# Optimization experiments

Measured on AMD Instinct MI355X. Metric: run time of the kernel, lower is better.

## Reference

```python
import jax, jax.numpy as jnp
import numpy as np

SEQ_LEN = 4096
N_FEAT = 2048
N_PADD = 128


def setup_inputs() -> dict:
    key = jax.random.key(0)
    kx, kw = jax.random.split(key)
    x = jax.random.normal(kx, (SEQ_LEN, N_FEAT), dtype=jnp.float32)
    # Fused QKV dense: features = 3 * n_feat
    W = jax.random.normal(kw, (N_FEAT, 3 * N_FEAT), dtype=jnp.float32) * (1.0 / np.sqrt(N_FEAT))
    b = jnp.zeros((3 * N_FEAT,), dtype=jnp.float32)
    return {"x": x, "W": W, "b": b, "n_padd": N_PADD}


def reference(x, W, b, n_padd):
    # Fused QKV projection, split along feature axis (as in nn.Dense + jnp.split)
    qkv = x @ W + b  # [S, 3F]
    q, k, v = jnp.split(qkv, 3, axis=1)  # each [S, F]
    S, F = q.shape
    idx = jnp.arange(S)
    # scores[i, j] = q_i . k_j / sqrt(F)
    scores = (q @ k.T) * (1.0 / jnp.sqrt(jnp.float32(F)))  # [S, S]
    seq_mask = idx >= n_padd                      # valid (non-padding) positions
    causal = idx[None, :] <= idx[:, None]         # j <= i
    mask = causal & seq_mask[None, :]             # kernel: causal_mask & seq_mask
    row_valid = seq_mask                          # rows < n_padd are not computed/stored
    neg_inf = jnp.float32(-jnp.inf)
    scores = jnp.where(mask, scores, neg_inf)
    # Fully-masked (padding) rows would softmax to NaN; neutralize then zero output.
    scores = jnp.where(row_valid[:, None], scores, 0.0)
    att = jax.nn.softmax(scores, axis=-1)         # row-wise stable softmax
    out = att @ v                                 # [S, F]
    out = jnp.where(row_valid[:, None], out, 0.0)  # padded rows produce zeros
    return out
```

## Files before the change

### kernel.cpp

```cpp
#include <hip/hip_runtime.h>
#include <cstdint>
#include <cstddef>

typedef unsigned short u16;
typedef short v8s __attribute__((ext_vector_type(8)));
typedef float v4f __attribute__((ext_vector_type(4)));

constexpr int SEQ = 4096;
constexpr int FEAT = 2048;
constexpr int F3 = 6144;


__device__ __forceinline__ u16 f2bf(float f) {
  union { float f; uint32_t u; } v; v.f = f;
  uint32_t r = v.u + 0x7FFFu + ((v.u >> 16) & 1u);
  return (u16)(r >> 16);
}

__device__ __forceinline__ float bf2f(u16 s) {
  union { uint32_t u; float f; } v; v.u = ((uint32_t)s) << 16;
  return v.f;
}

__device__ __forceinline__ void gld_lds16(const u16* g, u16* l) {
  __builtin_amdgcn_global_load_lds(
      (const __attribute__((address_space(1))) void*)g,
      (__attribute__((address_space(3))) void*)l, 16, 0, 0);
}


__global__ void cvt_f32_bf16(const float* __restrict__ in, u16* __restrict__ out, int n8) {
  int i = blockIdx.x * 256 + threadIdx.x;
  if (i >= n8) return;
  const float4* p = (const float4*)in + (size_t)i * 2;
  float4 a = p[0], b = p[1];
  union { u16 s[8]; uint4 v; } u;
  u.s[0] = f2bf(a.x); u.s[1] = f2bf(a.y); u.s[2] = f2bf(a.z); u.s[3] = f2bf(a.w);
  u.s[4] = f2bf(b.x); u.s[5] = f2bf(b.y); u.s[6] = f2bf(b.z); u.s[7] = f2bf(b.w);
  *(uint4*)(out + (size_t)i * 8) = u.v;
}

__global__ void transp_f2b(const float* __restrict__ in, int ldin,
                           u16* __restrict__ out, int ldout) {
  __shared__ float tile[32][33];
  int c0 = blockIdx.x * 32, r0 = blockIdx.y * 32;
  int tx = threadIdx.x, ty = threadIdx.y;
#pragma unroll
  for (int p = 0; p < 4; ++p)
    tile[ty + 8 * p][tx] = in[(size_t)(r0 + ty + 8 * p) * ldin + c0 + tx];
  __syncthreads();
#pragma unroll
  for (int p = 0; p < 4; ++p)
    out[(size_t)(c0 + ty + 8 * p) * ldout + r0 + tx] = f2bf(tile[tx][ty + 8 * p]);
}

__global__ void transp_b2b(const u16* __restrict__ in, int ldin,
                           u16* __restrict__ out, int ldout) {
  __shared__ u16 tile[32][33];
  int c0 = blockIdx.x * 32, r0 = blockIdx.y * 32;
  int tx = threadIdx.x, ty = threadIdx.y;
#pragma unroll
  for (int p = 0; p < 4; ++p)
    tile[ty + 8 * p][tx] = in[(size_t)(r0 + ty + 8 * p) * ldin + c0 + tx];
  __syncthreads();
#pragma unroll
  for (int p = 0; p < 4; ++p)
    out[(size_t)(c0 + ty + 8 * p) * ldout + r0 + tx] = tile[tx][ty + 8 * p];
}

template<int OUTBF, int ADDB, int MODE>
__global__ __launch_bounds__(256) void gemm_bt(
    const u16* __restrict__ A, int lda,
    const u16* __restrict__ B, int ldb,
    void* __restrict__ Cv, int ldc,
    int K, const float* __restrict__ bias, float scale) {
  int bi, bj, ks, ke;
  if (MODE == 1) {
    const int t = blockIdx.x;
    bi = (int)((sqrtf(8.f * t + 1.f) - 1.f) * 0.5f);
    while ((bi + 1) * (bi + 2) / 2 <= t) ++bi;
    while (bi * (bi + 1) / 2 > t) --bi;
    bj = t - bi * (bi + 1) / 2;
    const int half = K >> 1;
    ks = blockIdx.z * half; ke = ks + half;
    Cv = (void*)((u16*)Cv + (size_t)blockIdx.z * SEQ * SEQ);
  } else if (MODE == 2) {
    bi = blockIdx.y; bj = blockIdx.x;
    const int half = (bi + 1) * 64;
    ks = blockIdx.z * half; ke = ks + half;
  } else {
    bi = blockIdx.y; bj = blockIdx.x;
    ks = 0; ke = K;
  }
  const int i0 = bi * 128, j0 = bj * 128;

  __shared__ u16 As[128 * 64];
  __shared__ u16 Bs[128 * 64];

  const int t = threadIdx.x;
  const int w = t >> 6, l = t & 63;
  const int wr = w >> 1, wc = w & 1;
  const int lm = l & 15, lq = l >> 4;
  const int lqs = ((lq + (lm >> 1)) & 3) * 8;

  v4f acc[4][4];
#pragma unroll
  for (int a = 0; a < 4; ++a)
#pragma unroll
    for (int b = 0; b < 4; ++b)
      acc[a][b] = v4f{0.f, 0.f, 0.f, 0.f};

  const int c1 = t + 256;
  const int r0c = t >> 2, o0 = ((((t & 3) - ((t >> 3) & 3)) & 3)) * 8;
  const int r1c = c1 >> 2, o1 = ((((c1 & 3) - ((c1 >> 3) & 3)) & 3)) * 8;
  const u16* Ag0 = A + (size_t)(i0 + r0c) * lda + o0;
  const u16* Ag1 = A + (size_t)(i0 + r1c) * lda + o1;
  const u16* Bg0 = B + (size_t)(j0 + r0c) * ldb + o0;
  const u16* Bg1 = B + (size_t)(j0 + r1c) * ldb + o1;
  u16* Al0 = &As[w * 512];
  u16* Al1 = &As[w * 512 + 2048];
  u16* Bl0 = &Bs[w * 512];
  u16* Bl1 = &Bs[w * 512 + 2048];

  for (int k0 = ks; k0 < ke; k0 += 64) {
    gld_lds16(Ag0 + k0, Al0);
    gld_lds16(Ag1 + k0, Al1);
    gld_lds16(Bg0 + k0, Bl0);
    gld_lds16(Bg1 + k0, Bl1);
    gld_lds16(Ag0 + k0 + 32, Al0 + 4096);
    gld_lds16(Ag1 + k0 + 32, Al1 + 4096);
    gld_lds16(Bg0 + k0 + 32, Bl0 + 4096);
    gld_lds16(Bg1 + k0 + 32, Bl1 + 4096);
    __syncthreads();

#pragma unroll
    for (int s = 0; s < 2; ++s) {
      v8s af[4], bfr[4];
#pragma unroll
      for (int mi = 0; mi < 4; ++mi)
        af[mi] = *(const v8s*)&As[s * 4096 + (wr * 64 + mi * 16 + lm) * 32 + lqs];
#pragma unroll
      for (int ni = 0; ni < 4; ++ni)
        bfr[ni] = *(const v8s*)&Bs[s * 4096 + (wc * 64 + ni * 16 + lm) * 32 + lqs];
#pragma unroll
      for (int mi = 0; mi < 4; ++mi)
#pragma unroll
        for (int ni = 0; ni < 4; ++ni)
          acc[mi][ni] = __builtin_amdgcn_mfma_f32_16x16x32_bf16(af[mi], bfr[ni], acc[mi][ni], 0, 0, 0);
    }
    __syncthreads();
  }

#pragma unroll
  for (int mi = 0; mi < 4; ++mi) {
#pragma unroll
    for (int ni = 0; ni < 4; ++ni) {
      const int cc = j0 + wc * 64 + ni * 16 + lm;
      const float badd = ADDB ? bias[cc] : 0.f;
#pragma unroll
      for (int r = 0; r < 4; ++r) {
        const int rr = i0 + wr * 64 + mi * 16 + lq * 4 + r;
        float v = acc[mi][ni][r] * scale + badd;
        if (OUTBF)           ((u16*)Cv)[(size_t)rr * ldc + cc] = f2bf(v);
        else if (MODE == 2)  atomicAdd((float*)Cv + (size_t)rr * ldc + cc, v);
        else                 ((float*)Cv)[(size_t)rr * ldc + cc] = v;
      }
    }
  }
}

__global__ __launch_bounds__(256) void softmax_rows(
    const u16* __restrict__ S0, const u16* __restrict__ S1,
    u16* __restrict__ att, const int* __restrict__ npad_p) {
  const int i = blockIdx.x;
  const int np = *npad_p;
  const int kend = ((i >> 7) + 1) << 7;
  const u16* r0 = S0 + (size_t)i * SEQ;
  const u16* r1 = S1 + (size_t)i * SEQ;
  u16* arow = att + (size_t)i * SEQ;
  const int t = threadIdx.x;

  float m = -3.0e38f, s = 0.f;
  for (int j = np + t; j <= i; j += 256) {
    float v = bf2f(r0[j]) + bf2f(r1[j]);
    if (v > m) { s = s * __expf(m - v) + 1.f; m = v; }
    else       { s += __expf(v - m); }
  }
#pragma unroll
  for (int off = 32; off > 0; off >>= 1) {
    float mo = __shfl_xor(m, off);
    float so = __shfl_xor(s, off);
    float M = fmaxf(m, mo);
    s = s * __expf(m - M) + so * __expf(mo - M);
    m = M;
  }
  __shared__ float sm[4], ss[4];
  const int w = t >> 6, l = t & 63;
  if (l == 0) { sm[w] = m; ss[w] = s; }
  __syncthreads();
  const float M = fmaxf(fmaxf(sm[0], sm[1]), fmaxf(sm[2], sm[3]));
  const float Ssum = ss[0] * __expf(sm[0] - M) + ss[1] * __expf(sm[1] - M) +
                     ss[2] * __expf(sm[2] - M) + ss[3] * __expf(sm[3] - M);
  const float inv = 1.f / Ssum;

  for (int j0b = t * 8; j0b < kend; j0b += 2048) {
    union { u16 s8[8]; uint4 v; } u;
#pragma unroll
    for (int q = 0; q < 8; ++q) {
      const int j = j0b + q;
      float a = 0.f;
      if (j >= np && j <= i)
        a = __expf(bf2f(r0[j]) + bf2f(r1[j]) - M) * inv;
      u.s8[q] = f2bf(a);
    }
    *(uint4*)(arow + j0b) = u.v;
  }
}


extern "C" void kernel_launch(void* const* d_in, const int* in_sizes, int n_in,
                              void* d_out, int out_size, void* d_ws, size_t ws_size,
                              hipStream_t stream) {
  const float* x = (const float*)d_in[0];
  const float* W = (const float*)d_in[1];
  const float* b = (const float*)d_in[2];
  const int* npad = (const int*)d_in[3];
  float* out = (float*)d_out;

  char* p = (char*)d_ws;
  u16* xb = (u16*)p;
  u16* Wt = (u16*)(p + (size_t)SEQ * FEAT * 2);
  u16* att = (u16*)p;
  p += (size_t)SEQ * FEAT * 2 + (size_t)F3 * FEAT * 2;
  u16* qkvb = (u16*)p;  p += (size_t)SEQ * F3 * 2;
  u16* vt   = (u16*)p;  p += (size_t)FEAT * SEQ * 2;
  u16* sc0  = (u16*)p;  p += (size_t)SEQ * SEQ * 2;
  u16* sc1  = (u16*)p;  p += (size_t)SEQ * SEQ * 2;
  if (ws_size < (size_t)(p - (char*)d_ws)) return;

  const float scale = 0.02209708691207961f;

  hipMemsetAsync(d_out, 0, (size_t)SEQ * FEAT * sizeof(float), stream);

  cvt_f32_bf16<<<SEQ * FEAT / 8 / 256, 256, 0, stream>>>(x, xb, SEQ * FEAT / 8);
  transp_f2b<<<dim3(F3 / 32, FEAT / 32), dim3(32, 8), 0, stream>>>(W, F3, Wt, FEAT);
  gemm_bt<1, 1, 0><<<dim3(F3 / 128, SEQ / 128), 256, 0, stream>>>(
      xb, FEAT, Wt, FEAT, (void*)qkvb, F3, FEAT, b, 1.0f);
  transp_b2b<<<dim3(FEAT / 32, SEQ / 32), dim3(32, 8), 0, stream>>>(
      qkvb + 2 * FEAT, F3, vt, SEQ);
  gemm_bt<1, 0, 1><<<dim3(32 * 33 / 2, 1, 2), 256, 0, stream>>>(
      qkvb, F3, qkvb + FEAT, F3, (void*)sc0, SEQ, FEAT, nullptr, scale);
  softmax_rows<<<SEQ, 256, 0, stream>>>(sc0, sc1, att, npad);
  gemm_bt<0, 0, 2><<<dim3(FEAT / 128, SEQ / 128, 2), 256, 0, stream>>>(
      att, SEQ, vt, SEQ, (void*)out, FEAT, 0, nullptr, 1.0f);
}
```

Measured before the change: 410.2 us.

## Add 256x256 pipelined GEMM for QKV projection and full QK^T scores

Introduces a 512-thread 256x256-tile GEMM with double-buffered direct-to-LDS loads, interleaved barriers, MFMA priority raising and partial vmcnt waits. It replaces the 128-tile kernel for both the QKV projection and the score computation. The score GEMM now computes the full 4096x4096 square in one pass over K, instead of the lower-triangle tiles split into two K halves. That removes the second score buffer and the summing in softmax, at the cost of computing the masked upper triangle.

New measurement: 406.0 us. Within noise of the previous version (-1.0%).

```diff
diff --git a/kernel.cpp b/kernel.cpp
--- a/kernel.cpp
+++ b/kernel.cpp
@@ -75,16 +75,7 @@
     void* __restrict__ Cv, int ldc,
     int K, const float* __restrict__ bias, float scale) {
   int bi, bj, ks, ke;
-  if (MODE == 1) {
-    const int t = blockIdx.x;
-    bi = (int)((sqrtf(8.f * t + 1.f) - 1.f) * 0.5f);
-    while ((bi + 1) * (bi + 2) / 2 <= t) ++bi;
-    while (bi * (bi + 1) / 2 > t) --bi;
-    bj = t - bi * (bi + 1) / 2;
-    const int half = K >> 1;
-    ks = blockIdx.z * half; ke = ks + half;
-    Cv = (void*)((u16*)Cv + (size_t)blockIdx.z * SEQ * SEQ);
-  } else if (MODE == 2) {
+  if (MODE == 2) {
     bi = blockIdx.y; bj = blockIdx.x;
     const int half = (bi + 1) * 64;
     ks = blockIdx.z * half; ke = ks + half;
@@ -169,20 +160,161 @@
   }
 }
 
+
+#define BAR()   asm volatile("s_barrier" ::: "memory")
+#define LGKM0() asm volatile("s_waitcnt lgkmcnt(0)" ::: "memory")
+#define VMC6()  asm volatile("s_waitcnt vmcnt(6)" ::: "memory")
+
+#define LDA(BUF, MH) do { _Pragma("unroll") \
+  for (int fi = 0; fi < 4; ++fi) { \
+    const u16* ap = &As[BUF][wr][(MH) * 4096 + fi * 1024]; \
+    af[fi][0] = *(const v8s*)(ap + off0); \
+    af[fi][1] = *(const v8s*)(ap + off1); \
+  } } while (0)
+
+#define LDB(BUF) do { _Pragma("unroll") \
+  for (int ni = 0; ni < 4; ++ni) { \
+    const u16* bp = &Bs[BUF][bh][bo + ni * 1024]; \
+    bfr[ni][0] = *(const v8s*)(bp + off0); \
+    bfr[ni][1] = *(const v8s*)(bp + off1); \
+  } } while (0)
+
+#define MMA(MH, NL) do { _Pragma("unroll") \
+  for (int fi = 0; fi < 4; ++fi) { _Pragma("unroll") \
+    for (int nn = 0; nn < 2; ++nn) { \
+      acc[(MH)*4+fi][(NL)+nn] = __builtin_amdgcn_mfma_f32_16x16x32_bf16( \
+          af[fi][0], bfr[(NL)+nn][0], acc[(MH)*4+fi][(NL)+nn], 0, 0, 0); \
+      acc[(MH)*4+fi][(NL)+nn] = __builtin_amdgcn_mfma_f32_16x16x32_bf16( \
+          af[fi][1], bfr[(NL)+nn][1], acc[(MH)*4+fi][(NL)+nn], 0, 0, 0); \
+    } } } while (0)
+
+#define STG_A(BUF, H, KO) do { \
+  gld_lds16(Ag + (size_t)(H) * 128 * lda + (KO), &As[BUF][H][w * 1024]); \
+  gld_lds16(Ag + ((size_t)(H) * 128 + 8) * lda + (KO), &As[BUF][H][w * 1024 + 512]); \
+  } while (0)
+
+#define STG_B(BUF, H, KO) do { \
+  gld_lds16(Bg + (size_t)(H) * 128 * ldb + (KO), &Bs[BUF][H][w * 1024]); \
+  gld_lds16(Bg + ((size_t)(H) * 128 + 8) * ldb + (KO), &Bs[BUF][H][w * 1024 + 512]); \
+  } while (0)
+
+template<int ADDB>
+__global__ __launch_bounds__(512, 2) void gemm256(
+    const u16* __restrict__ A, int lda,
+    const u16* __restrict__ B, int ldb,
+    u16* __restrict__ C, int ldc,
+    int K, const float* __restrict__ bias, float scale) {
+  const int i0 = blockIdx.y * 256, j0 = blockIdx.x * 256;
+
+  __shared__ u16 As[2][2][8192];
+  __shared__ u16 Bs[2][2][8192];
+
+  const int t = threadIdx.x;
+  const int w = t >> 6, l = t & 63;
+  const int wr = w >> 2, wc = w & 3;
+  const int lm = l & 15, lq = l >> 4;
+  const int bh = wc >> 1, bo = (wc & 1) * 4096;
+
+  const int off0 = lm * 64 + ((lq + lm) & 7) * 8;
+  const int off1 = lm * 64 + ((lq + lm + 4) & 7) * 8;
+
+  const int srow = w * 16 + (l >> 3);
+  const int scol = (((l & 7) - (l >> 3)) & 7) * 8;
+  const u16* Ag = A + (size_t)(i0 + srow) * lda + scol;
+  const u16* Bg = B + (size_t)(j0 + srow) * ldb + scol;
+
+  v4f acc[8][4];
+#pragma unroll
+  for (int a = 0; a < 8; ++a)
+#pragma unroll
+    for (int b = 0; b < 4; ++b)
+      acc[a][b] = v4f{0.f, 0.f, 0.f, 0.f};
+
+  v8s af[4][2], bfr[4][2];
+
+  STG_B(0, 0, 0); STG_B(0, 1, 0); STG_A(0, 0, 0); STG_A(0, 1, 0);
+  STG_B(1, 0, 64); STG_B(1, 1, 64); STG_A(1, 0, 64);
+  VMC6(); BAR();
+
+  const int nit = K >> 7;
+  for (int it = 0; it < nit; ++it) {
+    const int kc = it << 7;
+    const int k1 = kc + 64;
+    int k2 = kc + 128; if (k2 >= K) k2 = 0;
+    int k3 = kc + 192; if (k3 >= K) k3 = 0;
+
+    LDA(0, 0); LDB(0);
+    STG_A(1, 1, k1);
+    BAR(); LGKM0();
+    __builtin_amdgcn_s_setprio(1); MMA(0, 0); __builtin_amdgcn_s_setprio(0);
+    BAR();
+    STG_B(0, 0, k2);
+    BAR();
+    __builtin_amdgcn_s_setprio(1); MMA(0, 2); __builtin_amdgcn_s_setprio(0);
+    BAR();
+    LDA(0, 1);
+    STG_B(0, 1, k2);
+    BAR(); LGKM0();
+    __builtin_amdgcn_s_setprio(1); MMA(1, 0); __builtin_amdgcn_s_setprio(0);
+    BAR();
+    STG_A(0, 0, k2);
+    BAR();
+    __builtin_amdgcn_s_setprio(1); MMA(1, 2); __builtin_amdgcn_s_setprio(0);
+    VMC6(); BAR();
+    LDA(1, 0); LDB(1);
+    STG_A(0, 1, k2);
+    BAR(); LGKM0();
+    __builtin_amdgcn_s_setprio(1); MMA(0, 0); __builtin_amdgcn_s_setprio(0);
+    BAR();
+    STG_B(1, 0, k3);
+    BAR();
+    __builtin_amdgcn_s_setprio(1); MMA(0, 2); __builtin_amdgcn_s_setprio(0);
+    BAR();
+    LDA(1, 1);
+    STG_B(1, 1, k3);
+    BAR(); LGKM0();
+    __builtin_amdgcn_s_setprio(1); MMA(1, 0); __builtin_amdgcn_s_setprio(0);
+    BAR();
+    STG_A(1, 0, k3);
+    BAR();
+    __builtin_amdgcn_s_setprio(1); MMA(1, 2); __builtin_amdgcn_s_setprio(0);
+    VMC6(); BAR();
+  }
+
+#pragma unroll
+  for (int mi = 0; mi < 8; ++mi) {
+#pragma unroll
+    for (int ni = 0; ni < 4; ++ni) {
+      const int cc = j0 + wc * 64 + ni * 16 + lm;
+      const float badd = ADDB ? bias[cc] : 0.f;
+#pragma unroll
+      for (int r = 0; r < 4; ++r) {
+        const int rr = i0 + wr * 128 + mi * 16 + lq * 4 + r;
+        C[(size_t)rr * ldc + cc] = f2bf(acc[mi][ni][r] * scale + badd);
+      }
+    }
+  }
+}
+
+#undef LDA
+#undef LDB
+#undef MMA
+#undef STG_A
+#undef STG_B
+
 __global__ __launch_bounds__(256) void softmax_rows(
-    const u16* __restrict__ S0, const u16* __restrict__ S1,
+    const u16* __restrict__ S0,
     u16* __restrict__ att, const int* __restrict__ npad_p) {
   const int i = blockIdx.x;
   const int np = *npad_p;
   const int kend = ((i >> 7) + 1) << 7;
   const u16* r0 = S0 + (size_t)i * SEQ;
-  const u16* r1 = S1 + (size_t)i * SEQ;
   u16* arow = att + (size_t)i * SEQ;
   const int t = threadIdx.x;
 
   float m = -3.0e38f, s = 0.f;
   for (int j = np + t; j <= i; j += 256) {
-    float v = bf2f(r0[j]) + bf2f(r1[j]);
+    float v = bf2f(r0[j]);
     if (v > m) { s = s * __expf(m - v) + 1.f; m = v; }
     else       { s += __expf(v - m); }
   }
@@ -210,7 +342,7 @@
       const int j = j0b + q;
       float a = 0.f;
       if (j >= np && j <= i)
-        a = __expf(bf2f(r0[j]) + bf2f(r1[j]) - M) * inv;
+        a = __expf(bf2f(r0[j]) - M) * inv;
       u.s8[q] = f2bf(a);
     }
     *(uint4*)(arow + j0b) = u.v;
@@ -235,7 +367,6 @@
   u16* qkvb = (u16*)p;  p += (size_t)SEQ * F3 * 2;
   u16* vt   = (u16*)p;  p += (size_t)FEAT * SEQ * 2;
   u16* sc0  = (u16*)p;  p += (size_t)SEQ * SEQ * 2;
-  u16* sc1  = (u16*)p;  p += (size_t)SEQ * SEQ * 2;
   if (ws_size < (size_t)(p - (char*)d_ws)) return;
 
   const float scale = 0.02209708691207961f;
@@ -244,13 +375,13 @@
 
   cvt_f32_bf16<<<SEQ * FEAT / 8 / 256, 256, 0, stream>>>(x, xb, SEQ * FEAT / 8);
   transp_f2b<<<dim3(F3 / 32, FEAT / 32), dim3(32, 8), 0, stream>>>(W, F3, Wt, FEAT);
-  gemm_bt<1, 1, 0><<<dim3(F3 / 128, SEQ / 128), 256, 0, stream>>>(
-      xb, FEAT, Wt, FEAT, (void*)qkvb, F3, FEAT, b, 1.0f);
+  gemm256<1><<<dim3(F3 / 256, SEQ / 256), 512, 0, stream>>>(
+      xb, FEAT, Wt, FEAT, qkvb, F3, FEAT, b, 1.0f);
   transp_b2b<<<dim3(FEAT / 32, SEQ / 32), dim3(32, 8), 0, stream>>>(
       qkvb + 2 * FEAT, F3, vt, SEQ);
-  gemm_bt<1, 0, 1><<<dim3(32 * 33 / 2, 1, 2), 256, 0, stream>>>(
-      qkvb, F3, qkvb + FEAT, F3, (void*)sc0, SEQ, FEAT, nullptr, scale);
-  softmax_rows<<<SEQ, 256, 0, stream>>>(sc0, sc1, att, npad);
+  gemm256<0><<<dim3(SEQ / 256, SEQ / 256), 512, 0, stream>>>(
+      qkvb, F3, qkvb + FEAT, F3, sc0, SEQ, FEAT, nullptr, scale);
+  softmax_rows<<<SEQ, 256, 0, stream>>>(sc0, att, npad);
   gemm_bt<0, 0, 2><<<dim3(FEAT / 128, SEQ / 128, 2), 256, 0, stream>>>(
       att, SEQ, vt, SEQ, (void*)out, FEAT, 0, nullptr, 1.0f);
 }
```

## Replace GEMM with 128x256 triple-buffered pipelined kernel and drop split-K scores

Applied to the files above, without the earlier changes.

The GEMM kernel is replaced by a 512-thread, 128x256-tile version. It uses a three-stage LDS ring buffer, issues the next global-to-LDS loads before the MFMAs, and waits with explicit vmcnt waits and barriers instead of full syncthreads. It also raises wave priority around the MFMA block and remaps workgroups with a swizzle. The score GEMM now computes the full square in one pass without triangle skipping or split-K, so softmax reads a single score buffer. The trade-off is roughly double the score GEMM work in exchange for better pipelining and larger tiles, and the causal PV split reverses row order across the two halves for balance.

New measurement: 410.1 us. No clear change (-0.0%).

```diff
diff --git a/kernel.cpp b/kernel.cpp
--- a/kernel.cpp
+++ b/kernel.cpp
@@ -68,87 +68,90 @@
     out[(size_t)(c0 + ty + 8 * p) * ldout + r0 + tx] = tile[tx][ty + 8 * p];
 }
 
-template<int OUTBF, int ADDB, int MODE>
-__global__ __launch_bounds__(256) void gemm_bt(
-    const u16* __restrict__ A, int lda,
-    const u16* __restrict__ B, int ldb,
-    void* __restrict__ Cv, int ldc,
-    int K, const float* __restrict__ bias, float scale) {
-  int bi, bj, ks, ke;
-  if (MODE == 1) {
-    const int t = blockIdx.x;
-    bi = (int)((sqrtf(8.f * t + 1.f) - 1.f) * 0.5f);
-    while ((bi + 1) * (bi + 2) / 2 <= t) ++bi;
-    while (bi * (bi + 1) / 2 > t) --bi;
-    bj = t - bi * (bi + 1) / 2;
-    const int half = K >> 1;
-    ks = blockIdx.z * half; ke = ks + half;
-    Cv = (void*)((u16*)Cv + (size_t)blockIdx.z * SEQ * SEQ);
-  } else if (MODE == 2) {
-    bi = blockIdx.y; bj = blockIdx.x;
-    const int half = (bi + 1) * 64;
-    ks = blockIdx.z * half; ke = ks + half;
-  } else {
-    bi = blockIdx.y; bj = blockIdx.x;
-    ks = 0; ke = K;
-  }
-  const int i0 = bi * 128, j0 = bj * 128;
-
-  __shared__ u16 As[128 * 64];
-  __shared__ u16 Bs[128 * 64];
+
+#define BAR()  asm volatile("s_barrier" ::: "memory")
+#define VMC3() asm volatile("s_waitcnt vmcnt(3)" ::: "memory")
+
+template<int LDA, int LDB, int LDC, int OUTMODE ,
+         int ADDB, int CAUSAL, int SWZ>
+__global__ __launch_bounds__(512, 4) void gemmw(
+    const u16* __restrict__ A, const u16* __restrict__ B,
+    void* __restrict__ Cv, int K,
+    const float* __restrict__ bias, float scale) {
+  int bi, bj;
+  if (SWZ) {
+    const int gx = gridDim.x;
+    const int nwg = gx * gridDim.y;
+    const int b = blockIdx.y * gx + blockIdx.x;
+    const int cpx = nwg >> 3;
+    const int s = (b & 7) * cpx + (b >> 3);
+    bj = s % gx;  bi = s / gx;
+  } else { bj = blockIdx.x; bi = blockIdx.y; }
+  int ks, ke;
+  if (CAUSAL) {
+    if (blockIdx.z) bi = (int)gridDim.y - 1 - bi;
+    const int kq = (bi + 1) * 64;
+    ks = blockIdx.z ? kq : 0;  ke = ks + kq;
+  } else { ks = 0; ke = K; }
+  const int i0 = bi * 128, j0 = bj * 256;
+
+  __shared__ u16 As[3][4096];
+  __shared__ u16 Bs[3][8192];
 
   const int t = threadIdx.x;
   const int w = t >> 6, l = t & 63;
-  const int wr = w >> 1, wc = w & 1;
+  const int wr = w >> 2, wc = w & 3;
   const int lm = l & 15, lq = l >> 4;
   const int lqs = ((lq + (lm >> 1)) & 3) * 8;
 
+  const int srow = t >> 2;
+  const int scol = (((t & 3) - ((t >> 3) & 3)) & 3) * 8;
+  const u16* Ag = A + (size_t)(i0 + srow) * LDA + scol;
+  const u16* Bg = B + (size_t)(j0 + srow) * LDB + scol;
+  u16* Al = &As[0][0] + w * 512;
+  u16* Bl = &Bs[0][0] + w * 512;
+
   v4f acc[4][4];
 #pragma unroll
   for (int a = 0; a < 4; ++a)
 #pragma unroll
-    for (int b = 0; b < 4; ++b)
-      acc[a][b] = v4f{0.f, 0.f, 0.f, 0.f};
-
-  const int c1 = t + 256;
-  const int r0c = t >> 2, o0 = ((((t & 3) - ((t >> 3) & 3)) & 3)) * 8;
-  const int r1c = c1 >> 2, o1 = ((((c1 & 3) - ((c1 >> 3) & 3)) & 3)) * 8;
-  const u16* Ag0 = A + (size_t)(i0 + r0c) * lda + o0;
-  const u16* Ag1 = A + (size_t)(i0 + r1c) * lda + o1;
-  const u16* Bg0 = B + (size_t)(j0 + r0c) * ldb + o0;
-  const u16* Bg1 = B + (size_t)(j0 + r1c) * ldb + o1;
-  u16* Al0 = &As[w * 512];
-  u16* Al1 = &As[w * 512 + 2048];
-  u16* Bl0 = &Bs[w * 512];
-  u16* Bl1 = &Bs[w * 512 + 2048];
-
-  for (int k0 = ks; k0 < ke; k0 += 64) {
-    gld_lds16(Ag0 + k0, Al0);
-    gld_lds16(Ag1 + k0, Al1);
-    gld_lds16(Bg0 + k0, Bl0);
-    gld_lds16(Bg1 + k0, Bl1);
-    gld_lds16(Ag0 + k0 + 32, Al0 + 4096);
-    gld_lds16(Ag1 + k0 + 32, Al1 + 4096);
-    gld_lds16(Bg0 + k0 + 32, Bl0 + 4096);
-    gld_lds16(Bg1 + k0 + 32, Bl1 + 4096);
-    __syncthreads();
-
-#pragma unroll
-    for (int s = 0; s < 2; ++s) {
-      v8s af[4], bfr[4];
-#pragma unroll
-      for (int mi = 0; mi < 4; ++mi)
-        af[mi] = *(const v8s*)&As[s * 4096 + (wr * 64 + mi * 16 + lm) * 32 + lqs];
+    for (int b2 = 0; b2 < 4; ++b2)
+      acc[a][b2] = v4f{0.f, 0.f, 0.f, 0.f};
+
+  gld_lds16(Ag + ks, Al);
+  gld_lds16(Bg + ks, Bl);
+  gld_lds16(Bg + 128 * LDB + ks, Bl + 4096);
+  gld_lds16(Ag + ks + 32, Al + 4096);
+  gld_lds16(Bg + ks + 32, Bl + 8192);
+  gld_lds16(Bg + 128 * LDB + ks + 32, Bl + 8192 + 4096);
+  VMC3(); BAR();
+
+  const int nt = (ke - ks) >> 5;
+  int bufr = 0;
+  int k2 = ks + 64;
+  for (int tt = 0; tt < nt; ++tt) {
+    v8s af[4], bf4[4];
+    const u16* Ar = &As[0][0] + bufr * 4096 + (wr * 64 + lm) * 32 + lqs;
+    const u16* Br = &Bs[0][0] + bufr * 8192 + (wc * 64 + lm) * 32 + lqs;
+#pragma unroll
+    for (int mi = 0; mi < 4; ++mi) af[mi] = *(const v8s*)(Ar + mi * 512);
+#pragma unroll
+    for (int ni = 0; ni < 4; ++ni) bf4[ni] = *(const v8s*)(Br + ni * 512);
+    const int sb = (bufr + 2 >= 3) ? bufr - 1 : bufr + 2;
+    const int kst = (k2 < ke) ? k2 : ks;
+    gld_lds16(Ag + kst, Al + sb * 4096);
+    gld_lds16(Bg + kst, Bl + sb * 8192);
+    gld_lds16(Bg + 128 * LDB + kst, Bl + sb * 8192 + 4096);
+    __builtin_amdgcn_s_setprio(1);
+#pragma unroll
+    for (int mi = 0; mi < 4; ++mi)
 #pragma unroll
       for (int ni = 0; ni < 4; ++ni)
-        bfr[ni] = *(const v8s*)&Bs[s * 4096 + (wc * 64 + ni * 16 + lm) * 32 + lqs];
-#pragma unroll
-      for (int mi = 0; mi < 4; ++mi)
-#pragma unroll
-        for (int ni = 0; ni < 4; ++ni)
-          acc[mi][ni] = __builtin_amdgcn_mfma_f32_16x16x32_bf16(af[mi], bfr[ni], acc[mi][ni], 0, 0, 0);
-    }
-    __syncthreads();
+        acc[mi][ni] = __builtin_amdgcn_mfma_f32_16x16x32_bf16(af[mi], bf4[ni], acc[mi][ni], 0, 0, 0);
+    __builtin_amdgcn_s_setprio(0);
+    VMC3(); BAR();
+    bufr = (bufr == 2) ? 0 : bufr + 1;
+    k2 += 32;
   }
 
 #pragma unroll
@@ -160,29 +163,28 @@
 #pragma unroll
       for (int r = 0; r < 4; ++r) {
         const int rr = i0 + wr * 64 + mi * 16 + lq * 4 + r;
-        float v = acc[mi][ni][r] * scale + badd;
-        if (OUTBF)           ((u16*)Cv)[(size_t)rr * ldc + cc] = f2bf(v);
-        else if (MODE == 2)  atomicAdd((float*)Cv + (size_t)rr * ldc + cc, v);
-        else                 ((float*)Cv)[(size_t)rr * ldc + cc] = v;
+        if (OUTMODE == 0)
+          ((u16*)Cv)[(size_t)rr * LDC + cc] = f2bf(acc[mi][ni][r] * scale + badd);
+        else
+          atomicAdd((float*)Cv + (size_t)rr * LDC + cc, acc[mi][ni][r]);
       }
     }
   }
 }
 
 __global__ __launch_bounds__(256) void softmax_rows(
-    const u16* __restrict__ S0, const u16* __restrict__ S1,
+    const u16* __restrict__ S0,
     u16* __restrict__ att, const int* __restrict__ npad_p) {
   const int i = blockIdx.x;
   const int np = *npad_p;
   const int kend = ((i >> 7) + 1) << 7;
   const u16* r0 = S0 + (size_t)i * SEQ;
-  const u16* r1 = S1 + (size_t)i * SEQ;
   u16* arow = att + (size_t)i * SEQ;
   const int t = threadIdx.x;
 
   float m = -3.0e38f, s = 0.f;
   for (int j = np + t; j <= i; j += 256) {
-    float v = bf2f(r0[j]) + bf2f(r1[j]);
+    float v = bf2f(r0[j]);
     if (v > m) { s = s * __expf(m - v) + 1.f; m = v; }
     else       { s += __expf(v - m); }
   }
@@ -210,7 +212,7 @@
       const int j = j0b + q;
       float a = 0.f;
       if (j >= np && j <= i)
-        a = __expf(bf2f(r0[j]) + bf2f(r1[j]) - M) * inv;
+        a = __expf(bf2f(r0[j]) - M) * inv;
       u.s8[q] = f2bf(a);
     }
     *(uint4*)(arow + j0b) = u.v;
@@ -235,7 +237,6 @@
   u16* qkvb = (u16*)p;  p += (size_t)SEQ * F3 * 2;
   u16* vt   = (u16*)p;  p += (size_t)FEAT * SEQ * 2;
   u16* sc0  = (u16*)p;  p += (size_t)SEQ * SEQ * 2;
-  u16* sc1  = (u16*)p;  p += (size_t)SEQ * SEQ * 2;
   if (ws_size < (size_t)(p - (char*)d_ws)) return;
 
   const float scale = 0.02209708691207961f;
@@ -244,13 +245,13 @@
 
   cvt_f32_bf16<<<SEQ * FEAT / 8 / 256, 256, 0, stream>>>(x, xb, SEQ * FEAT / 8);
   transp_f2b<<<dim3(F3 / 32, FEAT / 32), dim3(32, 8), 0, stream>>>(W, F3, Wt, FEAT);
-  gemm_bt<1, 1, 0><<<dim3(F3 / 128, SEQ / 128), 256, 0, stream>>>(
-      xb, FEAT, Wt, FEAT, (void*)qkvb, F3, FEAT, b, 1.0f);
+  gemmw<FEAT, FEAT, F3, 0, 1, 0, 1><<<dim3(F3 / 256, SEQ / 128), 512, 0, stream>>>(
+      xb, Wt, (void*)qkvb, FEAT, b, 1.0f);
   transp_b2b<<<dim3(FEAT / 32, SEQ / 32), dim3(32, 8), 0, stream>>>(
       qkvb + 2 * FEAT, F3, vt, SEQ);
-  gemm_bt<1, 0, 1><<<dim3(32 * 33 / 2, 1, 2), 256, 0, stream>>>(
-      qkvb, F3, qkvb + FEAT, F3, (void*)sc0, SEQ, FEAT, nullptr, scale);
-  softmax_rows<<<SEQ, 256, 0, stream>>>(sc0, sc1, att, npad);
-  gemm_bt<0, 0, 2><<<dim3(FEAT / 128, SEQ / 128, 2), 256, 0, stream>>>(
-      att, SEQ, vt, SEQ, (void*)out, FEAT, 0, nullptr, 1.0f);
-}
+  gemmw<F3, F3, SEQ, 0, 0, 0, 1><<<dim3(SEQ / 256, SEQ / 128), 512, 0, stream>>>(
+      qkvb, qkvb + FEAT, (void*)sc0, FEAT, nullptr, scale);
+  softmax_rows<<<SEQ, 256, 0, stream>>>(sc0, att, npad);
+  gemmw<SEQ, SEQ, FEAT, 1, 0, 1, 0><<<dim3(FEAT / 256, SEQ / 128, 2), 512, 0, stream>>>(
+      att, vt, (void*)out, 0, nullptr, 1.0f);
+}
```
